# Kernel optimization log

Measured on AMD Instinct MI355X. Metric: run time of the kernel, lower is better.

## Reference

```python
import jax, jax.numpy as jnp
import numpy as np

NUM_HEADS = 8  # matches init_kwargs num_heads
LN_EPS = 1e-5  # torch.nn.LayerNorm default


def setup_inputs() -> dict:
    key = jax.random.key(0)
    ks = jax.random.split(key, 12)
    E, B, H, S = 16384, 16, 256, 32
    edge_features = jax.random.normal(ks[0], (E, H), jnp.float32)
    edge_coords = jax.random.normal(ks[1], (E, 3), jnp.float32)
    # sorted, equal-size segments (all graphs non-empty)
    batch = jnp.repeat(jnp.arange(B, dtype=jnp.int32), E // B)
    s_h = 1.0 / np.sqrt(H)
    s_sh = 1.0 / np.sqrt(S * H)
    seed_vectors = jax.random.normal(ks[2], (S, H), jnp.float32)
    # weights stored [in, out] (transposed vs torch nn.Linear)
    Wq = jax.random.normal(ks[3], (H, H), jnp.float32) * s_h
    Wk = jax.random.normal(ks[4], (H, H), jnp.float32) * s_h
    Wv = jax.random.normal(ks[5], (H, H), jnp.float32) * s_h
    Wo = jax.random.normal(ks[6], (H, H), jnp.float32) * s_h
    bo = jnp.zeros((H,), jnp.float32)
    ln_g = jnp.ones((H,), jnp.float32)
    ln_b = jnp.zeros((H,), jnp.float32)
    W1 = jax.random.normal(ks[7], (S * H, H), jnp.float32) * s_sh
    b1 = jnp.zeros((H,), jnp.float32)
    W2 = jax.random.normal(ks[8], (H, H), jnp.float32) * s_h
    b2 = jnp.zeros((H,), jnp.float32)
    return dict(edge_features=edge_features, edge_coords=edge_coords, batch=batch,
                seed_vectors=seed_vectors, Wq=Wq, Wk=Wk, Wv=Wv, Wo=Wo, bo=bo,
                ln_g=ln_g, ln_b=ln_b, W1=W1, b1=b1, W2=W2, b2=b2, num_graphs=B)


def reference(edge_features, edge_coords, batch, seed_vectors, Wq, Wk, Wv, Wo, bo,
              ln_g, ln_b, W1, b1, W2, b2, num_graphs):
    S, H = seed_vectors.shape
    nh = NUM_HEADS
    hd = H // nh
    q = (seed_vectors @ Wq).reshape(S, nh, hd)          # shared across graphs
    k = (edge_features @ Wk).reshape(-1, nh, hd)        # [E, nh, hd]
    v = (edge_features @ Wv).reshape(-1, nh, hd)
    scores = jnp.einsum('shd,ehd->esh', q, k) / np.sqrt(hd).astype(np.float32)
    # segment softmax over edges within each graph
    m = jax.lax.stop_gradient(jax.ops.segment_max(scores, batch, num_segments=num_graphs))
    num = jnp.exp(scores - m[batch])
    den = jax.ops.segment_sum(num, batch, num_segments=num_graphs)
    w = num / den[batch]                                # [E, S, nh]
    att = jax.ops.segment_sum(jnp.einsum('esh,ehd->eshd', w, v), batch,
                              num_segments=num_graphs)  # [B, S, nh, hd]
    att = att.reshape(num_graphs, S, H)                 # concat heads (head-major)
    y = seed_vectors[None, :, :] + att @ Wo + bo        # residual + out_proj
    mu = jnp.mean(y, axis=-1, keepdims=True)
    var = jnp.mean((y - mu) ** 2, axis=-1, keepdims=True)
    y = (y - mu) / jnp.sqrt(var + LN_EPS) * ln_g + ln_b
    flat = y.reshape(num_graphs, S * H)
    h1 = jax.nn.silu(flat @ W1 + b1)
    return h1 @ W2 + b2                                 # [B, H]
```

## Files before the change

kernel.cpp:

```cpp
#include <hip/hip_runtime.h>
#include <math.h>
#include <stdint.h>

#define E_EDGES 16384
#define H_DIM   256
#define S_SEEDS 32
#define NHEADS  8
#define HDIM    32
#define BGRAPHS 16
#define EPG     1024
#define NCHUNK  256
#define CPG     16
#define RSQRT_HD 0.17677669529663687f

typedef __attribute__((ext_vector_type(8))) short bf16x8;
typedef __attribute__((ext_vector_type(4))) float f32x4;

__device__ inline unsigned short f2bf(float x) {
    unsigned u = __float_as_uint(x);
    u += 0x7fff + ((u >> 16) & 1);
    return (unsigned short)(u >> 16);
}
__device__ inline float bf2f(unsigned int h) {
    return __uint_as_float((h & 0xffffu) << 16);
}
__device__ inline unsigned pack2(float a, float b) {
    return (unsigned)f2bf(a) | ((unsigned)f2bf(b) << 16);
}

__global__ __launch_bounds__(256) void k_wc(const float* __restrict__ Wv,
                                            const float* __restrict__ Wk,
                                            const float* __restrict__ Wq,
                                            const float* __restrict__ seed,
                                            unsigned short* __restrict__ WcT) {
    int j = blockIdx.x;
    int i = threadIdx.x;
    float val;
    if (j < H_DIM) {
        val = Wv[i * H_DIM + j];
    } else {
        int c = j - H_DIM;
        int h = c >> 5, s = c & 31;
        __shared__ float qp[8][33];
        __shared__ float qrow[HDIM];
        int d = i & 31, g = i >> 5;
        const float* wq = &Wq[(g * 32) * H_DIM + h * HDIM + d];
        const float* sd = &seed[s * H_DIM + g * 32];
        float p = 0.f;
        #pragma unroll
        for (int ii = 0; ii < 32; ++ii)
            p = fmaf(sd[ii], wq[(size_t)ii * H_DIM], p);
        qp[g][d] = p;
        __syncthreads();
        if (i < HDIM) {
            float qv = 0.f;
            #pragma unroll
            for (int g2 = 0; g2 < 8; ++g2) qv += qp[g2][i];
            qrow[i] = qv;
        }
        __syncthreads();
        const float* wk = &Wk[i * H_DIM + h * HDIM];
        float acc = 0.f;
        #pragma unroll
        for (int dd = 0; dd < HDIM; dd += 4) {
            float4 w = *(const float4*)&wk[dd];
            float4 qq = *(const float4*)&qrow[dd];
            acc = fmaf(w.x, qq.x, acc); acc = fmaf(w.y, qq.y, acc);
            acc = fmaf(w.z, qq.z, acc); acc = fmaf(w.w, qq.w, acc);
        }
        val = acc * RSQRT_HD;
    }
    WcT[j * H_DIM + i] = f2bf(val);
}

struct SMattn {
    unsigned short As[64][264];
    unsigned short Vt[256][72];
    unsigned short Pt[256][72];
};

__global__ __launch_bounds__(512) void k_attn(const float* __restrict__ A,
                                              const unsigned short* __restrict__ WcT,
                                              float* __restrict__ outc,
                                              float* __restrict__ mg,
                                              float* __restrict__ sg) {
    __shared__ SMattn sm;
    int tid = threadIdx.x;
    int chunk = blockIdx.x;
    int e0 = chunk * 64;
    int w = tid >> 6, lane = tid & 63;
    int lr = lane & 15, kg = lane >> 4;

    {
        int r = tid >> 3, cg8 = tid & 7;
        const float* ap = &A[(size_t)(e0 + r) * H_DIM + cg8 * 32];
        #pragma unroll
        for (int i = 0; i < 4; ++i) {
            float4 x = *(const float4*)&ap[i * 8];
            float4 y = *(const float4*)&ap[i * 8 + 4];
            uint4 o;
            o.x = pack2(x.x, x.y); o.y = pack2(x.z, x.w);
            o.z = pack2(y.x, y.y); o.w = pack2(y.z, y.w);
            *(uint4*)&sm.As[r][cg8 * 32 + i * 8] = o;
        }
    }
    __syncthreads();

    const unsigned short* brow = &WcT[(size_t)(w * 64 + lr) * H_DIM + kg * 8];
    uint4 bfr[2][4];
    #pragma unroll
    for (int ni = 0; ni < 4; ++ni) {
        bfr[0][ni] = *(const uint4*)(brow + (size_t)ni * 16 * H_DIM);
        bfr[1][ni] = *(const uint4*)(brow + (size_t)ni * 16 * H_DIM + 32);
    }
    f32x4 acc[4][4] = {};
    #pragma unroll
    for (int k = 0; k < 8; ++k) {
        bf16x8 af[4], bv[4];
        #pragma unroll
        for (int mi = 0; mi < 4; ++mi)
            af[mi] = *(const bf16x8*)&sm.As[mi * 16 + lr][k * 32 + kg * 8];
        #pragma unroll
        for (int ni = 0; ni < 4; ++ni)
            bv[ni] = *(const bf16x8*)&bfr[k & 1][ni];
        if (k < 6) {
            #pragma unroll
            for (int ni = 0; ni < 4; ++ni)
                bfr[k & 1][ni] = *(const uint4*)(brow + (size_t)ni * 16 * H_DIM + (k + 2) * 32);
        }
        #pragma unroll
        for (int mi = 0; mi < 4; ++mi)
            #pragma unroll
            for (int ni = 0; ni < 4; ++ni)
                acc[mi][ni] = __builtin_amdgcn_mfma_f32_16x16x32_bf16(
                    af[mi], bv[ni], acc[mi][ni], 0, 0, 0);
    }

    if (w < 4) {
        #pragma unroll
        for (int mi = 0; mi < 4; ++mi)
            #pragma unroll
            for (int ni = 0; ni < 4; ++ni)
                #pragma unroll
                for (int r = 0; r < 4; ++r)
                    sm.Vt[w * 64 + ni * 16 + lr][mi * 16 + kg * 4 + r] =
                        f2bf(acc[mi][ni][r]);
    } else {
        int wn = (w - 4) * 64;
        #pragma unroll
        for (int ni = 0; ni < 4; ++ni) {
            float m = -1e30f;
            #pragma unroll
            for (int mi = 0; mi < 4; ++mi)
                #pragma unroll
                for (int r = 0; r < 4; ++r) m = fmaxf(m, acc[mi][ni][r]);
            m = fmaxf(m, __shfl_xor(m, 16, 64));
            m = fmaxf(m, __shfl_xor(m, 32, 64));
            float sv = 0.f;
            #pragma unroll
            for (int mi = 0; mi < 4; ++mi)
                #pragma unroll
                for (int r = 0; r < 4; ++r) {
                    float e_ = __expf(acc[mi][ni][r] - m);
                    unsigned short eb = f2bf(e_);
                    sm.Pt[wn + ni * 16 + lr][mi * 16 + kg * 4 + r] = eb;
                    sv += bf2f(eb);
                }
            sv += __shfl_xor(sv, 16, 64);
            sv += __shfl_xor(sv, 32, 64);
            if (kg == 0) {
                mg[(size_t)chunk * H_DIM + wn + ni * 16 + lr] = m;
                sg[(size_t)chunk * H_DIM + wn + ni * 16 + lr] = sv;
            }
        }
    }
    __syncthreads();

    f32x4 acc2[2][2] = {};
    #pragma unroll
    for (int ms = 0; ms < 2; ++ms)
        #pragma unroll
        for (int nd = 0; nd < 2; ++nd)
            #pragma unroll
            for (int kk = 0; kk < 2; ++kk) {
                bf16x8 pa = *(const bf16x8*)&sm.Pt[w * 32 + ms * 16 + lr][kk * 32 + kg * 8];
                bf16x8 vb = *(const bf16x8*)&sm.Vt[w * 32 + nd * 16 + lr][kk * 32 + kg * 8];
                acc2[ms][nd] = __builtin_amdgcn_mfma_f32_16x16x32_bf16(
                    pa, vb, acc2[ms][nd], 0, 0, 0);
            }
    #pragma unroll
    for (int ms = 0; ms < 2; ++ms)
        #pragma unroll
        for (int nd = 0; nd < 2; ++nd)
            #pragma unroll
            for (int r = 0; r < 4; ++r) {
                int s_ = ms * 16 + kg * 4 + r;
                int c_ = w * 32 + nd * 16 + lr;
                outc[((size_t)chunk * 32 + s_) * H_DIM + c_] = acc2[ms][nd][r];
            }
}

__device__ inline float block_sum256(float v, float* red4) {
    for (int o = 32; o > 0; o >>= 1) v += __shfl_xor(v, o, 64);
    int wid = threadIdx.x >> 6;
    if ((threadIdx.x & 63) == 0) red4[wid] = v;
    __syncthreads();
    float r = red4[0] + red4[1] + red4[2] + red4[3];
    __syncthreads();
    return r;
}

__global__ __launch_bounds__(256) void k_proj_ln(const float* __restrict__ outc,
                                                 const float* __restrict__ mg,
                                                 const float* __restrict__ sg,
                                                 const float* __restrict__ seed,
                                                 const float* __restrict__ Wo,
                                                 const float* __restrict__ bo,
                                                 const float* __restrict__ ln_g,
                                                 const float* __restrict__ ln_b,
                                                 float* __restrict__ Y) {
    int bs0 = blockIdx.x * 4;
    int c = threadIdx.x;
    int b = bs0 >> 5;
    __shared__ float sscale[4][CPG][8];
    __shared__ float arow[4][H_DIM];
    __shared__ float red4[4];
    if (c < 32) {
        int r = c >> 3, hh = c & 7;
        int s_r = (bs0 + r) & 31;
        int sc = hh * 32 + s_r;
        float mj[CPG];
        float M = -1e30f;
        #pragma unroll
        for (int j = 0; j < CPG; ++j) {
            mj[j] = mg[(size_t)(b * CPG + j) * H_DIM + sc];
            M = fmaxf(M, mj[j]);
        }
        float Den = 0.f;
        #pragma unroll
        for (int j = 0; j < CPG; ++j)
            Den += sg[(size_t)(b * CPG + j) * H_DIM + sc] * __expf(mj[j] - M);
        float inv = 1.f / Den;
        #pragma unroll
        for (int j = 0; j < CPG; ++j)
            sscale[r][j][hh] = __expf(mj[j] - M) * inv;
    }
    __syncthreads();
    int h = c >> 5;
    #pragma unroll
    for (int r = 0; r < 4; ++r) {
        int s_r = (bs0 + r) & 31;
        float a = 0.f;
        #pragma unroll
        for (int j = 0; j < CPG; ++j)
            a = fmaf(outc[((size_t)(b * CPG + j) * 32 + s_r) * H_DIM + c],
                     sscale[r][j][h], a);
        arow[r][c] = a;
    }
    __syncthreads();
    float acc[4];
    float b0 = bo[c];
    #pragma unroll
    for (int r = 0; r < 4; ++r) acc[r] = b0;
    for (int i = 0; i < H_DIM; i += 4) {
        float4 a0 = *(const float4*)&arow[0][i];
        float4 a1 = *(const float4*)&arow[1][i];
        float4 a2 = *(const float4*)&arow[2][i];
        float4 a3 = *(const float4*)&arow[3][i];
        float w0 = Wo[(i + 0) * H_DIM + c], w1 = Wo[(i + 1) * H_DIM + c];
        float w2 = Wo[(i + 2) * H_DIM + c], w3 = Wo[(i + 3) * H_DIM + c];
        acc[0] = fmaf(a0.x, w0, acc[0]); acc[0] = fmaf(a0.y, w1, acc[0]);
        acc[0] = fmaf(a0.z, w2, acc[0]); acc[0] = fmaf(a0.w, w3, acc[0]);
        acc[1] = fmaf(a1.x, w0, acc[1]); acc[1] = fmaf(a1.y, w1, acc[1]);
        acc[1] = fmaf(a1.z, w2, acc[1]); acc[1] = fmaf(a1.w, w3, acc[1]);
        acc[2] = fmaf(a2.x, w0, acc[2]); acc[2] = fmaf(a2.y, w1, acc[2]);
        acc[2] = fmaf(a2.z, w2, acc[2]); acc[2] = fmaf(a2.w, w3, acc[2]);
        acc[3] = fmaf(a3.x, w0, acc[3]); acc[3] = fmaf(a3.y, w1, acc[3]);
        acc[3] = fmaf(a3.z, w2, acc[3]); acc[3] = fmaf(a3.w, w3, acc[3]);
    }
    float g = ln_g[c], be = ln_b[c];
    #pragma unroll
    for (int r = 0; r < 4; ++r) {
        int bs = bs0 + r;
        float y = seed[(bs & 31) * H_DIM + c] + acc[r];
        float mu = block_sum256(y, red4) * (1.f / 256.f);
        float d = y - mu;
        float var = block_sum256(d * d, red4) * (1.f / 256.f);
        Y[(size_t)bs * H_DIM + c] = d * rsqrtf(var + 1e-5f) * g + be;
    }
}

__global__ __launch_bounds__(256) void k_mlp1(const float* __restrict__ Y,
                                              const float* __restrict__ W1,
                                              float* __restrict__ part) {
    int ch = blockIdx.x;
    int c = threadIdx.x;
    int i0 = ch * 64;
    __shared__ float fbuf[16][64];
    #pragma unroll
    for (int it = 0; it < 4; ++it) {
        int li = it * 256 + c;
        fbuf[li >> 6][li & 63] = Y[(size_t)(li >> 6) * 8192 + i0 + (li & 63)];
    }
    __syncthreads();
    float acc[16];
    #pragma unroll
    for (int b = 0; b < 16; ++b) acc[b] = 0.f;
    for (int ii = 0; ii < 64; ++ii) {
        float w = W1[(size_t)(i0 + ii) * H_DIM + c];
        #pragma unroll
        for (int b = 0; b < 16; ++b) acc[b] = fmaf(fbuf[b][ii], w, acc[b]);
    }
    #pragma unroll
    for (int b = 0; b < 16; ++b)
        part[((size_t)b * 128 + ch) * H_DIM + c] = acc[b];
}

__global__ __launch_bounds__(256) void k_mlp2(const float* __restrict__ part,
                                              const float* __restrict__ b1,
                                              const float* __restrict__ W2,
                                              const float* __restrict__ b2,
                                              float* __restrict__ out) {
    int b = blockIdx.x;
    int c = threadIdx.x;
    float s = b1[c];
    const float* pb = &part[(size_t)b * 128 * H_DIM + c];
    #pragma unroll 4
    for (int ch = 0; ch < 128; ++ch) s += pb[(size_t)ch * H_DIM];
    float h1 = s / (1.f + __expf(-s));
    __shared__ float hrow[H_DIM];
    hrow[c] = h1;
    __syncthreads();
    float acc = b2[c];
    for (int j = 0; j < H_DIM; j += 4) {
        float4 hq = *(const float4*)&hrow[j];
        acc = fmaf(hq.x, W2[(j + 0) * H_DIM + c], acc);
        acc = fmaf(hq.y, W2[(j + 1) * H_DIM + c], acc);
        acc = fmaf(hq.z, W2[(j + 2) * H_DIM + c], acc);
        acc = fmaf(hq.w, W2[(j + 3) * H_DIM + c], acc);
    }
    out[(size_t)b * H_DIM + c] = acc;
}

extern "C" void kernel_launch(void* const* d_in, const int* in_sizes, int n_in,
                              void* d_out, int out_size, void* d_ws, size_t ws_size,
                              hipStream_t stream) {
    const float* edge_features = (const float*)d_in[0];
    const float* seed = (const float*)d_in[3];
    const float* Wq   = (const float*)d_in[4];
    const float* Wk   = (const float*)d_in[5];
    const float* Wv   = (const float*)d_in[6];
    const float* Wo   = (const float*)d_in[7];
    const float* bo   = (const float*)d_in[8];
    const float* ln_g = (const float*)d_in[9];
    const float* ln_b = (const float*)d_in[10];
    const float* W1   = (const float*)d_in[11];
    const float* b1   = (const float*)d_in[12];
    const float* W2   = (const float*)d_in[13];
    const float* b2   = (const float*)d_in[14];
    float* out = (float*)d_out;

    float* ws = (float*)d_ws;
    unsigned short* WcT = (unsigned short*)ws;
    float* outc = ws + 65536;
    float* mg   = outc + 2097152;
    float* sg   = mg + 65536;
    float* Y    = sg + 65536;
    float* part = Y + 131072;

    k_wc      <<<512, 256, 0, stream>>>(Wv, Wk, Wq, seed, WcT);
    k_attn    <<<NCHUNK, 512, 0, stream>>>(edge_features, WcT, outc, mg, sg);
    k_proj_ln <<<BGRAPHS * S_SEEDS / 4, 256, 0, stream>>>(outc, mg, sg, seed, Wo, bo, ln_g, ln_b, Y);
    k_mlp1    <<<128, 256, 0, stream>>>(Y, W1, part);
    k_mlp2    <<<BGRAPHS, 256, 0, stream>>>(part, b1, W2, b2, out);
}
```

Baseline: 149.8 us.

## Fuse projection, LayerNorm and first MLP layer into one tail kernel

Merges k_proj_ln and k_mlp1 into a single k_tail kernel. Each block handles one seed for all 16 graphs and one quarter of the W1 output columns, so Wo rows are reused across 16 graphs and the normalized rows stay in shared memory instead of going through global memory. k_mlp2 now reduces 32 seed partials instead of 128 chunk partials. This removes one launch and the Y round-trip, but each of the four column-quarter blocks per seed recomputes the out-projection and LayerNorm, and the grid shrinks to 128 blocks.

```diff
diff --git a/kernel.cpp b/kernel.cpp
--- a/kernel.cpp
+++ b/kernel.cpp
@@ -200,35 +200,27 @@
             }
 }
 
-__device__ inline float block_sum256(float v, float* red4) {
-    for (int o = 32; o > 0; o >>= 1) v += __shfl_xor(v, o, 64);
-    int wid = threadIdx.x >> 6;
-    if ((threadIdx.x & 63) == 0) red4[wid] = v;
-    __syncthreads();
-    float r = red4[0] + red4[1] + red4[2] + red4[3];
-    __syncthreads();
-    return r;
-}
-
-__global__ __launch_bounds__(256) void k_proj_ln(const float* __restrict__ outc,
-                                                 const float* __restrict__ mg,
-                                                 const float* __restrict__ sg,
-                                                 const float* __restrict__ seed,
-                                                 const float* __restrict__ Wo,
-                                                 const float* __restrict__ bo,
-                                                 const float* __restrict__ ln_g,
-                                                 const float* __restrict__ ln_b,
-                                                 float* __restrict__ Y) {
-    int bs0 = blockIdx.x * 4;
+__global__ __launch_bounds__(256) void k_tail(const float* __restrict__ outc,
+                                              const float* __restrict__ mg,
+                                              const float* __restrict__ sg,
+                                              const float* __restrict__ seed,
+                                              const float* __restrict__ Wo,
+                                              const float* __restrict__ bo,
+                                              const float* __restrict__ ln_g,
+                                              const float* __restrict__ ln_b,
+                                              const float* __restrict__ W1,
+                                              float* __restrict__ part) {
+    int bx = blockIdx.x;
+    int s = bx >> 2, cq = bx & 3;
     int c = threadIdx.x;
-    int b = bs0 >> 5;
-    __shared__ float sscale[4][CPG][8];
-    __shared__ float arow[4][H_DIM];
-    __shared__ float red4[4];
-    if (c < 32) {
-        int r = c >> 3, hh = c & 7;
-        int s_r = (bs0 + r) & 31;
-        int sc = hh * 32 + s_r;
+    __shared__ float sscale[16][16][8];
+    __shared__ float arow[16][H_DIM];
+    __shared__ float ynorm[16][H_DIM];
+    __shared__ float wred[4][16];
+
+    if (c < 128) {
+        int b = c >> 3, h = c & 7;
+        int sc = h * 32 + s;
         float mj[CPG];
         float M = -1e30f;
         #pragma unroll
@@ -243,77 +235,86 @@
         float inv = 1.f / Den;
         #pragma unroll
         for (int j = 0; j < CPG; ++j)
-            sscale[r][j][hh] = __expf(mj[j] - M) * inv;
-    }
-    __syncthreads();
+            sscale[b][j][h] = __expf(mj[j] - M) * inv;
+    }
+    __syncthreads();
+
     int h = c >> 5;
-    #pragma unroll
-    for (int r = 0; r < 4; ++r) {
-        int s_r = (bs0 + r) & 31;
+    for (int b = 0; b < 16; ++b) {
         float a = 0.f;
         #pragma unroll
         for (int j = 0; j < CPG; ++j)
-            a = fmaf(outc[((size_t)(b * CPG + j) * 32 + s_r) * H_DIM + c],
-                     sscale[r][j][h], a);
-        arow[r][c] = a;
-    }
-    __syncthreads();
-    float acc[4];
-    float b0 = bo[c];
-    #pragma unroll
-    for (int r = 0; r < 4; ++r) acc[r] = b0;
-    for (int i = 0; i < H_DIM; i += 4) {
-        float4 a0 = *(const float4*)&arow[0][i];
-        float4 a1 = *(const float4*)&arow[1][i];
-        float4 a2 = *(const float4*)&arow[2][i];
-        float4 a3 = *(const float4*)&arow[3][i];
-        float w0 = Wo[(i + 0) * H_DIM + c], w1 = Wo[(i + 1) * H_DIM + c];
-        float w2 = Wo[(i + 2) * H_DIM + c], w3 = Wo[(i + 3) * H_DIM + c];
-        acc[0] = fmaf(a0.x, w0, acc[0]); acc[0] = fmaf(a0.y, w1, acc[0]);
-        acc[0] = fmaf(a0.z, w2, acc[0]); acc[0] = fmaf(a0.w, w3, acc[0]);
-        acc[1] = fmaf(a1.x, w0, acc[1]); acc[1] = fmaf(a1.y, w1, acc[1]);
-        acc[1] = fmaf(a1.z, w2, acc[1]); acc[1] = fmaf(a1.w, w3, acc[1]);
-        acc[2] = fmaf(a2.x, w0, acc[2]); acc[2] = fmaf(a2.y, w1, acc[2]);
-        acc[2] = fmaf(a2.z, w2, acc[2]); acc[2] = fmaf(a2.w, w3, acc[2]);
-        acc[3] = fmaf(a3.x, w0, acc[3]); acc[3] = fmaf(a3.y, w1, acc[3]);
-        acc[3] = fmaf(a3.z, w2, acc[3]); acc[3] = fmaf(a3.w, w3, acc[3]);
-    }
-    float g = ln_g[c], be = ln_b[c];
-    #pragma unroll
-    for (int r = 0; r < 4; ++r) {
-        int bs = bs0 + r;
-        float y = seed[(bs & 31) * H_DIM + c] + acc[r];
-        float mu = block_sum256(y, red4) * (1.f / 256.f);
-        float d = y - mu;
-        float var = block_sum256(d * d, red4) * (1.f / 256.f);
-        Y[(size_t)bs * H_DIM + c] = d * rsqrtf(var + 1e-5f) * g + be;
-    }
-}
-
-__global__ __launch_bounds__(256) void k_mlp1(const float* __restrict__ Y,
-                                              const float* __restrict__ W1,
-                                              float* __restrict__ part) {
-    int ch = blockIdx.x;
-    int c = threadIdx.x;
-    int i0 = ch * 64;
-    __shared__ float fbuf[16][64];
-    #pragma unroll
-    for (int it = 0; it < 4; ++it) {
-        int li = it * 256 + c;
-        fbuf[li >> 6][li & 63] = Y[(size_t)(li >> 6) * 8192 + i0 + (li & 63)];
-    }
-    __syncthreads();
-    float acc[16];
-    #pragma unroll
-    for (int b = 0; b < 16; ++b) acc[b] = 0.f;
-    for (int ii = 0; ii < 64; ++ii) {
-        float w = W1[(size_t)(i0 + ii) * H_DIM + c];
-        #pragma unroll
-        for (int b = 0; b < 16; ++b) acc[b] = fmaf(fbuf[b][ii], w, acc[b]);
-    }
-    #pragma unroll
-    for (int b = 0; b < 16; ++b)
-        part[((size_t)b * 128 + ch) * H_DIM + c] = acc[b];
+            a = fmaf(outc[((size_t)(b * CPG + j) * 32 + s) * H_DIM + c],
+                     sscale[b][j][h], a);
+        arow[b][c] = a;
+    }
+    __syncthreads();
+
+    float y[16];
+    {
+        float base = bo[c] + seed[s * H_DIM + c];
+        #pragma unroll
+        for (int b = 0; b < 16; ++b) y[b] = base;
+        for (int i = 0; i < H_DIM; i += 2) {
+            float w0 = Wo[(size_t)i * H_DIM + c];
+            float w1 = Wo[(size_t)(i + 1) * H_DIM + c];
+            #pragma unroll
+            for (int b = 0; b < 16; ++b) {
+                y[b] = fmaf(arow[b][i], w0, y[b]);
+                y[b] = fmaf(arow[b][i + 1], w1, y[b]);
+            }
+        }
+    }
+
+    {
+        int wid = c >> 6;
+        #pragma unroll
+        for (int b = 0; b < 16; ++b) {
+            float v = y[b];
+            #pragma unroll
+            for (int o = 32; o > 0; o >>= 1) v += __shfl_xor(v, o, 64);
+            if ((c & 63) == 0) wred[wid][b] = v;
+        }
+        __syncthreads();
+        float mu[16];
+        #pragma unroll
+        for (int b = 0; b < 16; ++b)
+            mu[b] = (wred[0][b] + wred[1][b] + wred[2][b] + wred[3][b]) * (1.f / 256.f);
+        __syncthreads();
+        #pragma unroll
+        for (int b = 0; b < 16; ++b) {
+            float d = y[b] - mu[b];
+            float v = d * d;
+            #pragma unroll
+            for (int o = 32; o > 0; o >>= 1) v += __shfl_xor(v, o, 64);
+            if ((c & 63) == 0) wred[wid][b] = v;
+        }
+        __syncthreads();
+        float g = ln_g[c], be = ln_b[c];
+        #pragma unroll
+        for (int b = 0; b < 16; ++b) {
+            float var = (wred[0][b] + wred[1][b] + wred[2][b] + wred[3][b]) * (1.f / 256.f);
+            ynorm[b][c] = (y[b] - mu[b]) * rsqrtf(var + 1e-5f) * g + be;
+        }
+    }
+    __syncthreads();
+
+    {
+        int cout = cq * 64 + (c & 63);
+        int bg = c >> 6;
+        float acc[4] = {0.f, 0.f, 0.f, 0.f};
+        const float* w1p = &W1[(size_t)(s * H_DIM) * H_DIM + cout];
+        for (int i = 0; i < H_DIM; ++i) {
+            float w = w1p[(size_t)i * H_DIM];
+            acc[0] = fmaf(ynorm[bg * 4 + 0][i], w, acc[0]);
+            acc[1] = fmaf(ynorm[bg * 4 + 1][i], w, acc[1]);
+            acc[2] = fmaf(ynorm[bg * 4 + 2][i], w, acc[2]);
+            acc[3] = fmaf(ynorm[bg * 4 + 3][i], w, acc[3]);
+        }
+        #pragma unroll
+        for (int k = 0; k < 4; ++k)
+            part[((size_t)s * BGRAPHS + bg * 4 + k) * H_DIM + cout] = acc[k];
+    }
 }
 
 __global__ __launch_bounds__(256) void k_mlp2(const float* __restrict__ part,
@@ -324,9 +325,9 @@
     int b = blockIdx.x;
     int c = threadIdx.x;
     float s = b1[c];
-    const float* pb = &part[(size_t)b * 128 * H_DIM + c];
-    #pragma unroll 4
-    for (int ch = 0; ch < 128; ++ch) s += pb[(size_t)ch * H_DIM];
+    #pragma unroll 8
+    for (int sc2 = 0; sc2 < 32; ++sc2)
+        s += part[((size_t)sc2 * BGRAPHS + b) * H_DIM + c];
     float h1 = s / (1.f + __expf(-s));
     __shared__ float hrow[H_DIM];
     hrow[c] = h1;
@@ -365,12 +366,10 @@
     float* outc = ws + 65536;
     float* mg   = outc + 2097152;
     float* sg   = mg + 65536;
-    float* Y    = sg + 65536;
-    float* part = Y + 131072;
-
-    k_wc      <<<512, 256, 0, stream>>>(Wv, Wk, Wq, seed, WcT);
-    k_attn    <<<NCHUNK, 512, 0, stream>>>(edge_features, WcT, outc, mg, sg);
-    k_proj_ln <<<BGRAPHS * S_SEEDS / 4, 256, 0, stream>>>(outc, mg, sg, seed, Wo, bo, ln_g, ln_b, Y);
-    k_mlp1    <<<128, 256, 0, stream>>>(Y, W1, part);
-    k_mlp2    <<<BGRAPHS, 256, 0, stream>>>(part, b1, W2, b2, out);
-}
+    float* part = sg + 65536;
+
+    k_wc   <<<512, 256, 0, stream>>>(Wv, Wk, Wq, seed, WcT);
+    k_attn <<<NCHUNK, 512, 0, stream>>>(edge_features, WcT, outc, mg, sg);
+    k_tail <<<128, 256, 0, stream>>>(outc, mg, sg, seed, Wo, bo, ln_g, ln_b, W1, part);
+    k_mlp2 <<<BGRAPHS, 256, 0, stream>>>(part, b1, W2, b2, out);
+}
```

Result: slower. 165.5 us (+10.5%).

## Spread tail kernels over more blocks for projection, MLP1, and MLP2

Applied to the files above, without the earlier changes.

The projection+LayerNorm kernel now handles one (graph, seed) row per block instead of four, giving 512 blocks instead of 128. The softmax-combine loads are parallelized across 128 threads. MLP1 is split into 512 blocks of 16 input rows each, with W1 loaded into registers. MLP2 uses 1024 threads to reduce the 512 partials and to split the W2 matvec. The aim is better GPU occupancy on these latency-bound small kernels. The cost is less reuse of Wo per block and four times more partial traffic between MLP1 and MLP2.

```diff
diff --git a/kernel.cpp b/kernel.cpp
--- a/kernel.cpp
+++ b/kernel.cpp
@@ -219,127 +219,110 @@
                                                  const float* __restrict__ ln_g,
                                                  const float* __restrict__ ln_b,
                                                  float* __restrict__ Y) {
-    int bs0 = blockIdx.x * 4;
+    int bs = blockIdx.x;
+    int b = bs >> 5, s = bs & 31;
     int c = threadIdx.x;
-    int b = bs0 >> 5;
-    __shared__ float sscale[4][CPG][8];
-    __shared__ float arow[4][H_DIM];
+    __shared__ float mjv[CPG][8], sgv[CPG][8], sscale[CPG][8];
+    __shared__ float arow[H_DIM];
     __shared__ float red4[4];
-    if (c < 32) {
-        int r = c >> 3, hh = c & 7;
-        int s_r = (bs0 + r) & 31;
-        int sc = hh * 32 + s_r;
-        float mj[CPG];
+    if (c < 128) {
+        int j = c >> 3, h = c & 7;
+        int sc = h * 32 + s;
+        mjv[j][h] = mg[(size_t)(b * CPG + j) * H_DIM + sc];
+        sgv[j][h] = sg[(size_t)(b * CPG + j) * H_DIM + sc];
+    }
+    __syncthreads();
+    if (c < 8) {
+        int h = c;
         float M = -1e30f;
         #pragma unroll
-        for (int j = 0; j < CPG; ++j) {
-            mj[j] = mg[(size_t)(b * CPG + j) * H_DIM + sc];
-            M = fmaxf(M, mj[j]);
-        }
+        for (int j = 0; j < CPG; ++j) M = fmaxf(M, mjv[j][h]);
         float Den = 0.f;
         #pragma unroll
+        for (int j = 0; j < CPG; ++j) Den += sgv[j][h] * __expf(mjv[j][h] - M);
+        float inv = 1.f / Den;
+        #pragma unroll
+        for (int j = 0; j < CPG; ++j) sscale[j][h] = __expf(mjv[j][h] - M) * inv;
+    }
+    __syncthreads();
+    {
+        int h = c >> 5;
+        float a = 0.f;
+        #pragma unroll
         for (int j = 0; j < CPG; ++j)
-            Den += sg[(size_t)(b * CPG + j) * H_DIM + sc] * __expf(mj[j] - M);
-        float inv = 1.f / Den;
-        #pragma unroll
-        for (int j = 0; j < CPG; ++j)
-            sscale[r][j][hh] = __expf(mj[j] - M) * inv;
-    }
-    __syncthreads();
-    int h = c >> 5;
-    #pragma unroll
-    for (int r = 0; r < 4; ++r) {
-        int s_r = (bs0 + r) & 31;
-        float a = 0.f;
-        #pragma unroll
-        for (int j = 0; j < CPG; ++j)
-            a = fmaf(outc[((size_t)(b * CPG + j) * 32 + s_r) * H_DIM + c],
-                     sscale[r][j][h], a);
-        arow[r][c] = a;
-    }
-    __syncthreads();
-    float acc[4];
-    float b0 = bo[c];
-    #pragma unroll
-    for (int r = 0; r < 4; ++r) acc[r] = b0;
-    for (int i = 0; i < H_DIM; i += 4) {
-        float4 a0 = *(const float4*)&arow[0][i];
-        float4 a1 = *(const float4*)&arow[1][i];
-        float4 a2 = *(const float4*)&arow[2][i];
-        float4 a3 = *(const float4*)&arow[3][i];
-        float w0 = Wo[(i + 0) * H_DIM + c], w1 = Wo[(i + 1) * H_DIM + c];
-        float w2 = Wo[(i + 2) * H_DIM + c], w3 = Wo[(i + 3) * H_DIM + c];
-        acc[0] = fmaf(a0.x, w0, acc[0]); acc[0] = fmaf(a0.y, w1, acc[0]);
-        acc[0] = fmaf(a0.z, w2, acc[0]); acc[0] = fmaf(a0.w, w3, acc[0]);
-        acc[1] = fmaf(a1.x, w0, acc[1]); acc[1] = fmaf(a1.y, w1, acc[1]);
-        acc[1] = fmaf(a1.z, w2, acc[1]); acc[1] = fmaf(a1.w, w3, acc[1]);
-        acc[2] = fmaf(a2.x, w0, acc[2]); acc[2] = fmaf(a2.y, w1, acc[2]);
-        acc[2] = fmaf(a2.z, w2, acc[2]); acc[2] = fmaf(a2.w, w3, acc[2]);
-        acc[3] = fmaf(a3.x, w0, acc[3]); acc[3] = fmaf(a3.y, w1, acc[3]);
-        acc[3] = fmaf(a3.z, w2, acc[3]); acc[3] = fmaf(a3.w, w3, acc[3]);
-    }
-    float g = ln_g[c], be = ln_b[c];
-    #pragma unroll
-    for (int r = 0; r < 4; ++r) {
-        int bs = bs0 + r;
-        float y = seed[(bs & 31) * H_DIM + c] + acc[r];
-        float mu = block_sum256(y, red4) * (1.f / 256.f);
-        float d = y - mu;
-        float var = block_sum256(d * d, red4) * (1.f / 256.f);
-        Y[(size_t)bs * H_DIM + c] = d * rsqrtf(var + 1e-5f) * g + be;
-    }
+            a = fmaf(outc[((size_t)(b * CPG + j) * 32 + s) * H_DIM + c],
+                     sscale[j][h], a);
+        arow[c] = a;
+    }
+    __syncthreads();
+    float y = bo[c] + seed[s * H_DIM + c];
+    #pragma unroll 4
+    for (int i = 0; i < H_DIM; ++i)
+        y = fmaf(arow[i], Wo[(size_t)i * H_DIM + c], y);
+    float mu = block_sum256(y, red4) * (1.f / 256.f);
+    float d = y - mu;
+    float var = block_sum256(d * d, red4) * (1.f / 256.f);
+    Y[(size_t)bs * H_DIM + c] = d * rsqrtf(var + 1e-5f) * ln_g[c] + ln_b[c];
 }
 
 __global__ __launch_bounds__(256) void k_mlp1(const float* __restrict__ Y,
                                               const float* __restrict__ W1,
                                               float* __restrict__ part) {
-    int ch = blockIdx.x;
+    int k = blockIdx.x;
     int c = threadIdx.x;
-    int i0 = ch * 64;
-    __shared__ float fbuf[16][64];
-    #pragma unroll
-    for (int it = 0; it < 4; ++it) {
-        int li = it * 256 + c;
-        fbuf[li >> 6][li & 63] = Y[(size_t)(li >> 6) * 8192 + i0 + (li & 63)];
-    }
-    __syncthreads();
+    int s_idx = k >> 4, io = (k & 15) * 16;
+    __shared__ float yl[16][17];
+    {
+        int b = c >> 4, ii = c & 15;
+        yl[b][ii] = Y[(size_t)(b * 32 + s_idx) * H_DIM + io + ii];
+    }
+    __syncthreads();
+    float w[16];
+    #pragma unroll
+    for (int ii = 0; ii < 16; ++ii)
+        w[ii] = W1[(size_t)(k * 16 + ii) * H_DIM + c];
     float acc[16];
     #pragma unroll
     for (int b = 0; b < 16; ++b) acc[b] = 0.f;
-    for (int ii = 0; ii < 64; ++ii) {
-        float w = W1[(size_t)(i0 + ii) * H_DIM + c];
-        #pragma unroll
-        for (int b = 0; b < 16; ++b) acc[b] = fmaf(fbuf[b][ii], w, acc[b]);
-    }
+    #pragma unroll
+    for (int ii = 0; ii < 16; ++ii)
+        #pragma unroll
+        for (int b = 0; b < 16; ++b)
+            acc[b] = fmaf(yl[b][ii], w[ii], acc[b]);
     #pragma unroll
     for (int b = 0; b < 16; ++b)
-        part[((size_t)b * 128 + ch) * H_DIM + c] = acc[b];
-}
-
-__global__ __launch_bounds__(256) void k_mlp2(const float* __restrict__ part,
-                                              const float* __restrict__ b1,
-                                              const float* __restrict__ W2,
-                                              const float* __restrict__ b2,
-                                              float* __restrict__ out) {
+        part[((size_t)b * 512 + k) * H_DIM + c] = acc[b];
+}
+
+__global__ __launch_bounds__(1024) void k_mlp2(const float* __restrict__ part,
+                                               const float* __restrict__ b1,
+                                               const float* __restrict__ W2,
+                                               const float* __restrict__ b2,
+                                               float* __restrict__ out) {
     int b = blockIdx.x;
-    int c = threadIdx.x;
-    float s = b1[c];
-    const float* pb = &part[(size_t)b * 128 * H_DIM + c];
+    int t = threadIdx.x;
+    int c = t & 255, g = t >> 8;
+    __shared__ float red[4][H_DIM];
+    __shared__ float hrow[H_DIM];
+    float sacc = 0.f;
+    const float* pb = &part[((size_t)b * 512 + g * 128) * H_DIM + c];
+    #pragma unroll 8
+    for (int ch = 0; ch < 128; ++ch) sacc += pb[(size_t)ch * H_DIM];
+    red[g][c] = sacc;
+    __syncthreads();
+    if (g == 0) {
+        float s = red[0][c] + red[1][c] + red[2][c] + red[3][c] + b1[c];
+        hrow[c] = s / (1.f + __expf(-s));
+    }
+    __syncthreads();
+    float wacc = 0.f;
     #pragma unroll 4
-    for (int ch = 0; ch < 128; ++ch) s += pb[(size_t)ch * H_DIM];
-    float h1 = s / (1.f + __expf(-s));
-    __shared__ float hrow[H_DIM];
-    hrow[c] = h1;
-    __syncthreads();
-    float acc = b2[c];
-    for (int j = 0; j < H_DIM; j += 4) {
-        float4 hq = *(const float4*)&hrow[j];
-        acc = fmaf(hq.x, W2[(j + 0) * H_DIM + c], acc);
-        acc = fmaf(hq.y, W2[(j + 1) * H_DIM + c], acc);
-        acc = fmaf(hq.z, W2[(j + 2) * H_DIM + c], acc);
-        acc = fmaf(hq.w, W2[(j + 3) * H_DIM + c], acc);
-    }
-    out[(size_t)b * H_DIM + c] = acc;
+    for (int j = g * 64; j < g * 64 + 64; ++j)
+        wacc = fmaf(hrow[j], W2[(size_t)j * H_DIM + c], wacc);
+    red[g][c] = wacc;
+    __syncthreads();
+    if (g == 0)
+        out[(size_t)b * H_DIM + c] = red[0][c] + red[1][c] + red[2][c] + red[3][c] + b2[c];
 }
 
 extern "C" void kernel_launch(void* const* d_in, const int* in_sizes, int n_in,
@@ -370,7 +353,7 @@
 
     k_wc      <<<512, 256, 0, stream>>>(Wv, Wk, Wq, seed, WcT);
     k_attn    <<<NCHUNK, 512, 0, stream>>>(edge_features, WcT, outc, mg, sg);
-    k_proj_ln <<<BGRAPHS * S_SEEDS / 4, 256, 0, stream>>>(outc, mg, sg, seed, Wo, bo, ln_g, ln_b, Y);
-    k_mlp1    <<<128, 256, 0, stream>>>(Y, W1, part);
-    k_mlp2    <<<BGRAPHS, 256, 0, stream>>>(part, b1, W2, b2, out);
-}
+    k_proj_ln <<<512, 256, 0, stream>>>(outc, mg, sg, seed, Wo, bo, ln_g, ln_b, Y);
+    k_mlp1    <<<512, 256, 0, stream>>>(Y, W1, part);
+    k_mlp2    <<<BGRAPHS, 1024, 0, stream>>>(part, b1, W2, b2, out);
+}
```

Result: no change. 150.4 us (+0.4%).
